# Performance work log

Measured on AMD Instinct MI355X. Metric: run time of the kernel, lower is better.

The kernel has to match this reference:

```python
import jax, jax.numpy as jnp
import numpy as np

RESO = 64
PAD = 0.1
SCALE = 8.0
PLANES = {'xz': (0, 2), 'xy': (0, 1), 'yz': (1, 2)}
PLANE_ORDER = ['xz', 'xy', 'yz']


def normalize_coordinate(p, plane):
    i, j = PLANES[plane]
    xy = jnp.stack([p[..., i], p[..., j]], axis=-1)
    xy = xy / (1.0 + PAD + 1e-3) + 0.5
    return jnp.clip(xy, 0.0, 1.0 - 1e-5)


def coordinate2index(xy, reso):
    x = (xy * reso).astype(jnp.int32)
    return x[..., 0] + reso * x[..., 1]  # (B, T)


def resblock(x, W0, b0, W1, b1, Ws):
    # ResnetBlockFC: fc_1(relu(fc_0(relu(x)))) + shortcut(x)
    net = jnp.maximum(x, 0.0) @ W0 + b0
    dx = jnp.maximum(net, 0.0) @ W1 + b1
    return x @ Ws + dx


def scatter_max_pool(c, idx_flat, num_seg):
    # c: (B, T, h); idx_flat: (B*T,) batch-offset plane indices
    B, T, h = c.shape
    pooled = jax.ops.segment_max(c.reshape(B * T, h), idx_flat, num_segments=num_seg)
    return pooled[idx_flat].reshape(B, T, h)


def plane_feature(p, c, plane):
    # scatter_mean of c into (B, c_dim, RESO, RESO); empty cells -> 0
    B, T, cd = c.shape
    R2 = RESO * RESO
    idx = coordinate2index(normalize_coordinate(p / SCALE, plane), RESO)
    idxf = (idx + jnp.arange(B, dtype=jnp.int32)[:, None] * R2).reshape(-1)
    sums = jax.ops.segment_sum(c.reshape(B * T, cd), idxf, num_segments=B * R2)
    cnt = jax.ops.segment_sum(jnp.ones((B * T,), c.dtype), idxf, num_segments=B * R2)
    mean = sums / jnp.maximum(cnt, 1.0)[:, None]
    return mean.reshape(B, R2, cd).transpose(0, 2, 1).reshape(B, cd, RESO, RESO)


def forward(p, fc_pos_W, fc_pos_b, blocks_W0, blocks_b0, blocks_W1, blocks_b1, blocks_Ws, fc_c_W, fc_c_b):
    B, T, _ = p.shape
    R2 = RESO * RESO
    offs = jnp.arange(B, dtype=jnp.int32)[:, None] * R2
    idx = {k: (coordinate2index(normalize_coordinate(p / SCALE, k), RESO) + offs).reshape(-1)
           for k in PLANE_ORDER}

    net = p @ fc_pos_W + fc_pos_b  # (B, T, 3h)
    net = resblock(net, blocks_W0[0], blocks_b0[0], blocks_W1[0], blocks_b1[0], blocks_Ws[0])
    n_blocks = blocks_W0.shape[0]
    for i in range(1, n_blocks):
        pooled = sum(scatter_max_pool(net, idx[k], B * R2) for k in PLANE_ORDER)
        meanp = jnp.broadcast_to(net.mean(axis=1, keepdims=True), net.shape)
        net = jnp.concatenate([net, pooled, meanp], axis=-1)  # (B, T, 3h)
        net = resblock(net, blocks_W0[i], blocks_b0[i], blocks_W1[i], blocks_b1[i], blocks_Ws[i])

    c = net @ fc_c_W + fc_c_b  # (B, T, c_dim)
    fea = jnp.stack([plane_feature(p, c, k) for k in PLANE_ORDER], axis=0)
    return fea  # (3, B, c_dim, RESO, RESO) in order xz, xy, yz


def setup_inputs() -> dict:
    key = jax.random.key(0)
    ks = jax.random.split(key, 10)
    B, T, dim = 16, 8192, 3
    h, c_dim, nb = 128, 128, 5
    s = 0.05
    return {
        'p': jax.random.normal(ks[0], (B, T, dim), jnp.float32) * 2.0,
        'fc_pos_W': jax.random.normal(ks[1], (dim, 3 * h), jnp.float32) * s,
        'fc_pos_b': jnp.zeros((3 * h,), jnp.float32),
        'blocks_W0': jax.random.normal(ks[2], (nb, 3 * h, h), jnp.float32) * s,
        'blocks_b0': jnp.zeros((nb, h), jnp.float32),
        'blocks_W1': jax.random.normal(ks[3], (nb, h, h), jnp.float32) * s,
        'blocks_b1': jnp.zeros((nb, h), jnp.float32),
        'blocks_Ws': jax.random.normal(ks[4], (nb, 3 * h, h), jnp.float32) * s,
        'fc_c_W': jax.random.normal(ks[5], (h, c_dim), jnp.float32) * s,
        'fc_c_b': jnp.zeros((c_dim,), jnp.float32),
    }


def reference(p, fc_pos_W, fc_pos_b, blocks_W0, blocks_b0, blocks_W1, blocks_b1, blocks_Ws, fc_c_W, fc_c_b):
    return forward(p, fc_pos_W, fc_pos_b, blocks_W0, blocks_b0, blocks_W1, blocks_b1, blocks_Ws, fc_c_W, fc_c_b)
```

## Files before the change

### kernel.cpp

```cpp
#include <hip/hip_runtime.h>

#define BT (16 * 8192)
#define NB 5
#define NCELL 65536
typedef unsigned int uint;
typedef unsigned short ushort;
typedef __attribute__((ext_vector_type(8))) short bf16x8;
typedef __attribute__((ext_vector_type(4))) float f32x4;


__device__ __forceinline__ uint f2bf(float x) {
    uint u = __float_as_uint(x);
    return (u + 0x7fffu + ((u >> 16) & 1u)) >> 16;
}
__device__ __forceinline__ float bf2f_lo(uint u) { return __uint_as_float(u << 16); }
__device__ __forceinline__ float bf2f_hi(uint u) { return __uint_as_float(u & 0xffff0000u); }
__device__ __forceinline__ uint pack2(float a, float b) { return f2bf(a) | (f2bf(b) << 16); }

__device__ __forceinline__ uint relu2(uint u) {
    uint m = (u >> 15) & 0x00010001u;
    return u & ~(m * 0xffffu);
}
__device__ __forceinline__ bf16x8 relu8(bf16x8 a) {
    uint4 u = *(uint4*)&a;
    u.x = relu2(u.x); u.y = relu2(u.y); u.z = relu2(u.z); u.w = relu2(u.w);
    return *(bf16x8*)&u;
}
__device__ __forceinline__ f32x4 bcast4(float x) { return (f32x4){x, x, x, x}; }
__device__ __forceinline__ f32x4 mfma16(bf16x8 a, bf16x8 b, f32x4 c) {
    return __builtin_amdgcn_mfma_f32_16x16x32_bf16(a, b, c, 0, 0, 0);
}

__global__ void k_idx(const float* __restrict__ p, int* __restrict__ idx) {
    int r = blockIdx.x * 256 + threadIdx.x;
    if (r >= BT) return;
    float p0 = p[3 * r + 0], p1 = p[3 * r + 1], p2 = p[3 * r + 2];
    const float DEN = (float)(1.0 + 0.1 + 1e-3);
    const float HI  = (float)(1.0 - 1e-5);
    int b = r >> 13;
    float x0 = fminf(fmaxf((p0 / 8.0f) / DEN + 0.5f, 0.0f), HI);
    float x1 = fminf(fmaxf((p1 / 8.0f) / DEN + 0.5f, 0.0f), HI);
    float x2 = fminf(fmaxf((p2 / 8.0f) / DEN + 0.5f, 0.0f), HI);
    int i0 = (int)(x0 * 64.0f);
    int i1 = (int)(x1 * 64.0f);
    int i2 = (int)(x2 * 64.0f);
    int base = b << 12;
    idx[r]          = base + i0 + (i2 << 6);
    idx[BT + r]     = base + i0 + (i1 << 6);
    idx[2 * BT + r] = base + i1 + (i2 << 6);
}

__global__ void k_hist(const int* __restrict__ idx, int* __restrict__ cnt) {
    int r = blockIdx.x * 256 + threadIdx.x;
    if (r >= BT) return;
    atomicAdd(cnt + idx[r], 1);
    atomicAdd(cnt + NCELL + idx[BT + r], 1);
    atomicAdd(cnt + 2 * NCELL + idx[2 * BT + r], 1);
}

__global__ __launch_bounds__(1024) void k_scan(const int* __restrict__ cnt,
                                               int* __restrict__ starts,
                                               int* __restrict__ cursor) {
    __shared__ int sc[1024];
    int pl = blockIdx.x, t = threadIdx.x;
    const int* c = cnt + pl * NCELL;
    int base = t * 64;
    int s = 0;
    for (int i = 0; i < 64; ++i) s += c[base + i];
    sc[t] = s;
    __syncthreads();
    for (int off = 1; off < 1024; off <<= 1) {
        int v = (t >= off) ? sc[t - off] : 0;
        __syncthreads();
        sc[t] += v;
        __syncthreads();
    }
    int run = sc[t] - s;
    for (int i = 0; i < 64; ++i) {
        int cell = base + i;
        starts[pl * NCELL + cell] = run;
        cursor[pl * NCELL + cell] = run;
        run += c[cell];
    }
}

__global__ void k_scatter_order(const int* __restrict__ idx, int* __restrict__ cursor,
                                int* __restrict__ order) {
    int r = blockIdx.x * 256 + threadIdx.x;
    if (r >= BT) return;
    for (int pl = 0; pl < 3; ++pl) {
        int cell = idx[pl * BT + r];
        int pos = atomicAdd(cursor + pl * NCELL + cell, 1);
        order[pl * BT + pos] = r;
    }
}

__global__ void k_wconv(const float* __restrict__ W0, const float* __restrict__ W1,
                        const float* __restrict__ Ws, const float* __restrict__ Wc,
                        ushort* __restrict__ wb) {
    int mat = blockIdx.y;
    int K = (mat < 5 || (mat >= 10 && mat < 15)) ? 384 : 128;
    int e = blockIdx.x * 256 + threadIdx.x;
    if (e >= K * 128) return;
    const float* src;
    size_t doff;
    if (mat < 5)       { src = W0 + (size_t)mat * 49152;        doff = (size_t)mat * 49152; }
    else if (mat < 10) { src = W1 + (size_t)(mat - 5) * 16384;  doff = 245760 + (size_t)(mat - 5) * 16384; }
    else if (mat < 15) { src = Ws + (size_t)(mat - 10) * 49152; doff = 327680 + (size_t)(mat - 10) * 49152; }
    else               { src = Wc;                              doff = 573440; }
    int ko = e & 31, n = (e >> 5) & 127, kt = e >> 12;
    wb[doff + e] = (ushort)f2bf(src[(size_t)(kt * 32 + ko) * 128 + n]);
}

__global__ __launch_bounds__(128) void k_meanvec(const float* __restrict__ meanB,
                                                 const ushort* __restrict__ wb0,
                                                 const float* __restrict__ b0v,
                                                 const ushort* __restrict__ wbs,
                                                 const float* __restrict__ b1v,
                                                 float* __restrict__ rv0,
                                                 float* __restrict__ rvS) {
    __shared__ float ms[128];
    int b = blockIdx.x, n = threadIdx.x;
    ms[n] = meanB[b * 128 + n];
    __syncthreads();
    float s0 = b0v[n], ss = b1v[n];
#pragma unroll 4
    for (int k = 0; k < 128; ++k) {
        float mv = ms[k];
        int kt = 8 + (k >> 5), ko = k & 31;
        float w0 = bf2f_lo((uint)wb0[kt * 4096 + n * 32 + ko]);
        float ws = bf2f_lo((uint)wbs[kt * 4096 + n * 32 + ko]);
        s0 = fmaf(fmaxf(mv, 0.0f), w0, s0);
        ss = fmaf(mv, ws, ss);
    }
    rv0[b * 128 + n] = s0;
    rvS[b * 128 + n] = ss;
}

__global__ __launch_bounds__(256) void k_segmax(const uint* __restrict__ netu,
                                                const int* __restrict__ starts,
                                                const int* __restrict__ cnt,
                                                const int* __restrict__ order,
                                                uint* __restrict__ segu) {
    int g = blockIdx.x * 4 + (threadIdx.x >> 6);
    int l = threadIdx.x & 63;
    int n = cnt[g];
    if (n == 0) return;
    int pl = g >> 16;
    const int* ord = order + pl * BT + starts[g];
    float m0 = -INFINITY, m1 = -INFINITY;
    int i = 0;
    for (; i + 4 <= n; i += 4) {
        uint a = netu[(size_t)ord[i] * 64 + l];
        uint b = netu[(size_t)ord[i + 1] * 64 + l];
        uint c = netu[(size_t)ord[i + 2] * 64 + l];
        uint d = netu[(size_t)ord[i + 3] * 64 + l];
        m0 = fmaxf(fmaxf(m0, fmaxf(bf2f_lo(a), bf2f_lo(b))), fmaxf(bf2f_lo(c), bf2f_lo(d)));
        m1 = fmaxf(fmaxf(m1, fmaxf(bf2f_hi(a), bf2f_hi(b))), fmaxf(bf2f_hi(c), bf2f_hi(d)));
    }
    int rem = n - i;
    if (rem > 0) {
        uint a = netu[(size_t)ord[i] * 64 + l];
        uint b = (rem > 1) ? netu[(size_t)ord[i + 1] * 64 + l] : a;
        uint c = (rem > 2) ? netu[(size_t)ord[i + 2] * 64 + l] : a;
        m0 = fmaxf(m0, fmaxf(bf2f_lo(a), fmaxf(bf2f_lo(b), bf2f_lo(c))));
        m1 = fmaxf(m1, fmaxf(bf2f_hi(a), fmaxf(bf2f_hi(b), bf2f_hi(c))));
    }
    segu[(size_t)g * 64 + l] = pack2(m0, m1);
}

template <int MODE>
__global__ __launch_bounds__(512, 6) void k_resblock(
    const float* __restrict__ p, const uint* __restrict__ netu,
    const int* __restrict__ idxg, const ushort* __restrict__ seg,
    const float* __restrict__ rv0, const float* __restrict__ rvS,
    const float* __restrict__ Wp, const float* __restrict__ bp,
    const ushort* __restrict__ wb0, const float* __restrict__ b0v,
    const ushort* __restrict__ wb1, const float* __restrict__ b1v,
    const ushort* __restrict__ wbs,
    ushort* __restrict__ out, float* __restrict__ meanW) {
    constexpr int LDA = (MODE == 0) ? 392 : 264;
    constexpr int NKT = (MODE == 0) ? 12 : 8;
    __shared__ __align__(16) ushort aT[64 * LDA];
    __shared__ __align__(16) ushort hT[64 * 136];
    const int t = threadIdx.x;
    const int rowBase = blockIdx.x * 64;
    const int bb = rowBase >> 13;

    if constexpr (MODE == 0) {
        for (int f = t; f < 3072; f += 512) {
            int row = f / 48, g = f - row * 48;
            const float* pr = p + (size_t)(rowBase + row) * 3;
            float p0 = pr[0], p1 = pr[1], p2 = pr[2];
            int k0 = g * 8;
            uint d[4];
#pragma unroll
            for (int w = 0; w < 4; ++w) {
                int k = k0 + 2 * w;
                float v0 = bp[k]     + p0 * Wp[k]     + p1 * Wp[384 + k]     + p2 * Wp[768 + k];
                float v1 = bp[k + 1] + p0 * Wp[k + 1] + p1 * Wp[384 + k + 1] + p2 * Wp[768 + k + 1];
                d[w] = pack2(v0, v1);
            }
            *(uint4*)(aT + row * LDA + k0) = make_uint4(d[0], d[1], d[2], d[3]);
        }
    } else {
        const uint4* nsrc = (const uint4*)netu;
#pragma unroll
        for (int i = 0; i < 2; ++i) {
            int f = t + 512 * i;
            int row = f >> 4, cu = f & 15;
            *(uint4*)(aT + row * LDA + cu * 8) = nsrc[(size_t)(rowBase + row) * 16 + cu];
        }
#pragma unroll
        for (int i = 0; i < 2; ++i) {
            int f = t + 512 * i;
            int row = f >> 4, grp = f & 15;
            int prow = rowBase + row;
            float o[8] = {};
#pragma unroll
            for (int pl = 0; pl < 3; ++pl) {
                int cell = idxg[pl * BT + prow];
                uint4 s4 = *(const uint4*)(seg + (size_t)(pl * NCELL + cell) * 128 + grp * 8);
                o[0] += bf2f_lo(s4.x); o[1] += bf2f_hi(s4.x);
                o[2] += bf2f_lo(s4.y); o[3] += bf2f_hi(s4.y);
                o[4] += bf2f_lo(s4.z); o[5] += bf2f_hi(s4.z);
                o[6] += bf2f_lo(s4.w); o[7] += bf2f_hi(s4.w);
            }
            uint4 d = make_uint4(pack2(o[0], o[1]), pack2(o[2], o[3]),
                                 pack2(o[4], o[5]), pack2(o[6], o[7]));
            *(uint4*)(aT + row * LDA + 128 + grp * 8) = d;
        }
    }
    __syncthreads();

    const int l = t & 63, wid = t >> 6;
    const int n0 = wid * 16;
    const int lm = l & 15, lg = l >> 4;
    const ushort* w0 = wb0 + n0 * 32;
    const ushort* w1 = wb1 + n0 * 32;
    const ushort* ws = wbs + n0 * 32;

    f32x4 acc0[4], accS[4];
    {
        float bi, si;
        if constexpr (MODE == 0) { bi = b0v[n0 + lm];            si = b1v[n0 + lm]; }
        else                     { bi = rv0[bb * 128 + n0 + lm]; si = rvS[bb * 128 + n0 + lm]; }
#pragma unroll
        for (int im = 0; im < 4; ++im) { acc0[im] = bcast4(bi); accS[im] = bcast4(si); }
    }
#pragma unroll
    for (int kt = 0; kt < NKT; ++kt) {
        bf16x8 b0 = *(const bf16x8*)(w0 + kt * 4096 + lm * 32 + lg * 8);
        bf16x8 bs = *(const bf16x8*)(ws + kt * 4096 + lm * 32 + lg * 8);
#pragma unroll
        for (int im = 0; im < 4; ++im) {
            bf16x8 a = *(const bf16x8*)(aT + (im * 16 + lm) * LDA + kt * 32 + lg * 8);
            acc0[im] = mfma16(relu8(a), b0, acc0[im]);
            accS[im] = mfma16(a, bs, accS[im]);
        }
    }
#pragma unroll
    for (int im = 0; im < 4; ++im)
#pragma unroll
        for (int j = 0; j < 4; ++j) {
            int row = im * 16 + lg * 4 + j;
            hT[row * 136 + n0 + lm] = (ushort)f2bf(fmaxf(acc0[im][j], 0.0f));
        }
    __syncthreads();

#pragma unroll
    for (int kt = 0; kt < 4; ++kt) {
        bf16x8 b = *(const bf16x8*)(w1 + kt * 4096 + lm * 32 + lg * 8);
#pragma unroll
        for (int im = 0; im < 4; ++im) {
            bf16x8 a = *(const bf16x8*)(hT + (im * 16 + lm) * 136 + kt * 32 + lg * 8);
            accS[im] = mfma16(a, b, accS[im]);
        }
    }

#pragma unroll
    for (int im = 0; im < 4; ++im)
#pragma unroll
        for (int j = 0; j < 4; ++j) {
            int row = rowBase + im * 16 + lg * 4 + j;
            out[(size_t)row * 128 + n0 + lm] = (ushort)f2bf(accS[im][j]);
        }

    if (meanW) {
        float s = 0.0f;
#pragma unroll
        for (int im = 0; im < 4; ++im)
#pragma unroll
            for (int j = 0; j < 4; ++j) s += accS[im][j];
        s += __shfl_xor(s, 16);
        s += __shfl_xor(s, 32);
        if (l < 16) atomicAdd(meanW + bb * 128 + n0 + l, s * (1.0f / 8192.0f));
    }
}

__device__ __forceinline__ void mfma_gemm3(const ushort* __restrict__ aLDS, int lda, int nk,
                                           const ushort* __restrict__ wb, int lm, int lg,
                                           f32x4 acc[4][2]) {
    for (int kt = 0; kt < nk; ++kt) {
        bf16x8 b0 = *(const bf16x8*)(wb + kt * 4096 + lm * 32 + lg * 8);
        bf16x8 b1 = *(const bf16x8*)(wb + kt * 4096 + (16 + lm) * 32 + lg * 8);
#pragma unroll
        for (int im = 0; im < 4; ++im) {
            bf16x8 a = *(const bf16x8*)(aLDS + (im * 16 + lm) * lda + kt * 32 + lg * 8);
            acc[im][0] = mfma16(a, b0, acc[im][0]);
            acc[im][1] = mfma16(a, b1, acc[im][1]);
        }
    }
}

__global__ __launch_bounds__(256, 2) void k_fcc(const uint* __restrict__ netu,
                                                const ushort* __restrict__ wbc,
                                                const float* __restrict__ bc,
                                                ushort* __restrict__ cout) {
    __shared__ __align__(16) ushort aT[64 * 136];
    const int t = threadIdx.x;
    const int rowBase = blockIdx.x * 64;
    const uint4* nsrc = (const uint4*)netu;
#pragma unroll
    for (int i = 0; i < 4; ++i) {
        int u = t + 256 * i;
        int row = u >> 4, cu = u & 15;
        *(uint4*)(aT + row * 136 + cu * 8) = nsrc[(size_t)(rowBase + row) * 16 + cu];
    }
    __syncthreads();
    const int l = t & 63, wid = t >> 6;
    const int n0 = wid * 32;
    const int lm = l & 15, lg = l >> 4;
    f32x4 acc[4][2];
    {
        float ci0 = bc[n0 + lm], ci1 = bc[n0 + 16 + lm];
#pragma unroll
        for (int im = 0; im < 4; ++im) { acc[im][0] = bcast4(ci0); acc[im][1] = bcast4(ci1); }
    }
    mfma_gemm3(aT, 136, 4, wbc + n0 * 32, lm, lg, acc);
#pragma unroll
    for (int im = 0; im < 4; ++im)
#pragma unroll
        for (int ic = 0; ic < 2; ++ic)
#pragma unroll
            for (int j = 0; j < 4; ++j) {
                int row = rowBase + im * 16 + lg * 4 + j;
                int col = n0 + ic * 16 + lm;
                cout[(size_t)row * 128 + col] = (ushort)f2bf(acc[im][ic][j]);
            }
}

__global__ __launch_bounds__(256) void k_segsum(const uint* __restrict__ cp,
                                                const int* __restrict__ starts,
                                                const int* __restrict__ cnt,
                                                const int* __restrict__ order,
                                                float* __restrict__ sums, int pl) {
    int cell = blockIdx.x * 4 + (threadIdx.x >> 6);
    int l = threadIdx.x & 63;
    int n = cnt[pl * NCELL + cell];
    if (n == 0) return;
    const int* ord = order + pl * BT + starts[pl * NCELL + cell];
    float s0 = 0.f, s1 = 0.f;
    int i = 0;
    for (; i + 4 <= n; i += 4) {
        uint a = cp[(size_t)ord[i] * 64 + l];
        uint b = cp[(size_t)ord[i + 1] * 64 + l];
        uint c = cp[(size_t)ord[i + 2] * 64 + l];
        uint d = cp[(size_t)ord[i + 3] * 64 + l];
        s0 += (bf2f_lo(a) + bf2f_lo(b)) + (bf2f_lo(c) + bf2f_lo(d));
        s1 += (bf2f_hi(a) + bf2f_hi(b)) + (bf2f_hi(c) + bf2f_hi(d));
    }
    int rem = n - i;
    if (rem > 0) {
        uint a = cp[(size_t)ord[i] * 64 + l];
        uint b = (rem > 1) ? cp[(size_t)ord[i + 1] * 64 + l] : 0u;
        uint c = (rem > 2) ? cp[(size_t)ord[i + 2] * 64 + l] : 0u;
        s0 += bf2f_lo(a) + (bf2f_lo(b) + bf2f_lo(c));
        s1 += bf2f_hi(a) + (bf2f_hi(b) + bf2f_hi(c));
    }
    *(float2*)(sums + (size_t)cell * 128 + 2 * l) = make_float2(s0, s1);
}

__global__ __launch_bounds__(256) void k_fin(const float* __restrict__ sums,
                                             const int* __restrict__ cnt,
                                             float* __restrict__ out, int pl) {
    __shared__ float tile[32][33];
    int t = threadIdx.x;
    int tx = t & 31, ty = t >> 5;
    int cl0 = (blockIdx.x & 127) << 5;
    int ch0 = (blockIdx.x >> 7) << 5;
    int b = blockIdx.y;
    int bc = b << 12;
#pragma unroll
    for (int j = 0; j < 4; ++j)
        tile[ty + 8 * j][tx] = sums[(size_t)(bc + cl0 + ty + 8 * j) * 128 + ch0 + tx];
    __syncthreads();
#pragma unroll
    for (int j = 0; j < 4; ++j) {
        int ch = ch0 + ty + 8 * j;
        int cl = cl0 + tx;
        int cn = cnt[pl * NCELL + bc + cl];
        float v = cn > 0 ? tile[tx][ty + 8 * j] / (float)cn : 0.0f;
        out[((size_t)((pl * 16 + b) * 128 + ch) << 12) + cl] = v;
    }
}

extern "C" void kernel_launch(void* const* d_in, const int* in_sizes, int n_in,
                              void* d_out, int out_size, void* d_ws, size_t ws_size,
                              hipStream_t stream) {
    const float* p  = (const float*)d_in[0];
    const float* Wp = (const float*)d_in[1];
    const float* bp = (const float*)d_in[2];
    const float* W0 = (const float*)d_in[3];
    const float* b0 = (const float*)d_in[4];
    const float* W1 = (const float*)d_in[5];
    const float* b1 = (const float*)d_in[6];
    const float* Ws = (const float*)d_in[7];
    const float* Wc = (const float*)d_in[8];
    const float* bc = (const float*)d_in[9];
    float* out = (float*)d_out;

    ushort* net    = (ushort*)d_ws;
    ushort* seg    = net + 16777216;
    float*  sums   = (float*)seg;
    ushort* wb     = seg + 25165824;
    int*    idx    = (int*)(wb + 589824);
    int*    order  = idx + 393216;
    int*    cnt    = order + 393216;
    int*    starts = cnt + 196608;
    int*    cursor = starts + 196608;
    float*  meanB  = (float*)(cursor + 196608);
    float*  rv0    = meanB + 2 * 2048;
    float*  rvS    = rv0 + 2048;

    k_idx<<<512, 256, 0, stream>>>(p, idx);
    hipMemsetAsync(cnt, 0, 3 * NCELL * 4, stream);
    k_hist<<<512, 256, 0, stream>>>(idx, cnt);
    k_scan<<<3, 1024, 0, stream>>>(cnt, starts, cursor);
    k_scatter_order<<<512, 256, 0, stream>>>(idx, cursor, order);
    k_wconv<<<dim3(192, 16), 256, 0, stream>>>(W0, W1, Ws, Wc, wb);

    hipMemsetAsync(meanB, 0, 2048 * 4, stream);
    k_resblock<0><<<2048, 512, 0, stream>>>(
        p, nullptr, nullptr, nullptr, nullptr, nullptr, Wp, bp,
        wb, b0, wb + 245760, b1, wb + 327680, net, meanB);

    for (int i = 1; i < NB; ++i) {
        const ushort* wb0i = wb + (size_t)i * 49152;
        const ushort* wb1i = wb + 245760 + (size_t)i * 16384;
        const ushort* wbsi = wb + 327680 + (size_t)i * 49152;
        k_segmax<<<49152, 256, 0, stream>>>((const uint*)net, starts, cnt, order, (uint*)seg);
        k_meanvec<<<16, 128, 0, stream>>>(meanB + ((i - 1) & 1) * 2048,
                                          wb0i, b0 + i * 128, wbsi, b1 + i * 128, rv0, rvS);
        float* mw = nullptr;
        if (i < NB - 1) {
            mw = meanB + (i & 1) * 2048;
            hipMemsetAsync(mw, 0, 2048 * 4, stream);
        }
        k_resblock<1><<<2048, 512, 0, stream>>>(
            nullptr, (const uint*)net, idx, seg, rv0, rvS, nullptr, nullptr,
            wb0i, nullptr, wb1i, nullptr, wbsi, net, mw);
    }

    k_fcc<<<2048, 256, 0, stream>>>((const uint*)net, wb + 573440, bc, net);

    for (int pl = 0; pl < 3; ++pl) {
        k_segsum<<<16384, 256, 0, stream>>>((const uint*)net, starts, cnt, order, sums, pl);
        k_fin<<<dim3(512, 16), 256, 0, stream>>>(sums, cnt, out, pl);
    }
}
```

Before: 765.1 us.

## Switch activations and weights from bf16 to fp16 with packed half ops

Replaces bf16 storage and MFMA with fp16 (16x16x32 f16 MFMA) throughout. This lets the segment-max and pooled-gather sum use packed v_pk_max_f16 and v_pk_add_f16 instead of unpacking to float and repacking. It also adds an interleaved int4 index array so the resblock gather loads all three plane cells with one 16-byte load. The trade-off is fp16's narrower range and round-toward-zero conversion, which may lose accuracy or overflow, plus an extra index write in k_idx.

After: 767.8 us. Within noise of the previous version (+0.3%).

```diff
diff --git a/kernel.cpp b/kernel.cpp
--- a/kernel.cpp
+++ b/kernel.cpp
@@ -5,33 +5,41 @@
 #define NCELL 65536
 typedef unsigned int uint;
 typedef unsigned short ushort;
-typedef __attribute__((ext_vector_type(8))) short bf16x8;
+typedef __attribute__((ext_vector_type(8))) _Float16 half8;
+typedef __attribute__((ext_vector_type(2))) __fp16 fp16x2;
+typedef __attribute__((ext_vector_type(2))) _Float16 half2v;
 typedef __attribute__((ext_vector_type(4))) float f32x4;
 
 
-__device__ __forceinline__ uint f2bf(float x) {
-    uint u = __float_as_uint(x);
-    return (u + 0x7fffu + ((u >> 16) & 1u)) >> 16;
-}
-__device__ __forceinline__ float bf2f_lo(uint u) { return __uint_as_float(u << 16); }
-__device__ __forceinline__ float bf2f_hi(uint u) { return __uint_as_float(u & 0xffff0000u); }
-__device__ __forceinline__ uint pack2(float a, float b) { return f2bf(a) | (f2bf(b) << 16); }
+__device__ __forceinline__ uint f2h2(float a, float b) {
+    fp16x2 h = __builtin_amdgcn_cvt_pkrtz(a, b);
+    return *(uint*)&h;
+}
+__device__ __forceinline__ float h2f_lo(uint u) { half2v h = *(half2v*)&u; return (float)h[0]; }
+__device__ __forceinline__ float h2f_hi(uint u) { half2v h = *(half2v*)&u; return (float)h[1]; }
+__device__ __forceinline__ uint pk_add(uint a, uint b) {
+    uint d; asm("v_pk_add_f16 %0, %1, %2" : "=v"(d) : "v"(a), "v"(b)); return d;
+}
+__device__ __forceinline__ uint pk_max(uint a, uint b) {
+    uint d; asm("v_pk_max_f16 %0, %1, %2" : "=v"(d) : "v"(a), "v"(b)); return d;
+}
 
 __device__ __forceinline__ uint relu2(uint u) {
     uint m = (u >> 15) & 0x00010001u;
     return u & ~(m * 0xffffu);
 }
-__device__ __forceinline__ bf16x8 relu8(bf16x8 a) {
+__device__ __forceinline__ half8 relu8(half8 a) {
     uint4 u = *(uint4*)&a;
     u.x = relu2(u.x); u.y = relu2(u.y); u.z = relu2(u.z); u.w = relu2(u.w);
-    return *(bf16x8*)&u;
+    return *(half8*)&u;
 }
 __device__ __forceinline__ f32x4 bcast4(float x) { return (f32x4){x, x, x, x}; }
-__device__ __forceinline__ f32x4 mfma16(bf16x8 a, bf16x8 b, f32x4 c) {
-    return __builtin_amdgcn_mfma_f32_16x16x32_bf16(a, b, c, 0, 0, 0);
-}
-
-__global__ void k_idx(const float* __restrict__ p, int* __restrict__ idx) {
+__device__ __forceinline__ f32x4 mfma16(half8 a, half8 b, f32x4 c) {
+    return __builtin_amdgcn_mfma_f32_16x16x32_f16(a, b, c, 0, 0, 0);
+}
+
+__global__ void k_idx(const float* __restrict__ p, int* __restrict__ idx,
+                      int4* __restrict__ idx4) {
     int r = blockIdx.x * 256 + threadIdx.x;
     if (r >= BT) return;
     float p0 = p[3 * r + 0], p1 = p[3 * r + 1], p2 = p[3 * r + 2];
@@ -45,9 +53,11 @@
     int i1 = (int)(x1 * 64.0f);
     int i2 = (int)(x2 * 64.0f);
     int base = b << 12;
-    idx[r]          = base + i0 + (i2 << 6);
-    idx[BT + r]     = base + i0 + (i1 << 6);
-    idx[2 * BT + r] = base + i1 + (i2 << 6);
+    int exz = base + i0 + (i2 << 6);
+    int exy = base + i0 + (i1 << 6);
+    int eyz = base + i1 + (i2 << 6);
+    idx[r] = exz; idx[BT + r] = exy; idx[2 * BT + r] = eyz;
+    idx4[r] = make_int4(exz, exy, eyz, 0);
 }
 
 __global__ void k_hist(const int* __restrict__ idx, int* __restrict__ cnt) {
@@ -109,7 +119,7 @@
     else if (mat < 15) { src = Ws + (size_t)(mat - 10) * 49152; doff = 327680 + (size_t)(mat - 10) * 49152; }
     else               { src = Wc;                              doff = 573440; }
     int ko = e & 31, n = (e >> 5) & 127, kt = e >> 12;
-    wb[doff + e] = (ushort)f2bf(src[(size_t)(kt * 32 + ko) * 128 + n]);
+    wb[doff + e] = (ushort)f2h2(src[(size_t)(kt * 32 + ko) * 128 + n], 0.0f);
 }
 
 __global__ __launch_bounds__(128) void k_meanvec(const float* __restrict__ meanB,
@@ -128,8 +138,8 @@
     for (int k = 0; k < 128; ++k) {
         float mv = ms[k];
         int kt = 8 + (k >> 5), ko = k & 31;
-        float w0 = bf2f_lo((uint)wb0[kt * 4096 + n * 32 + ko]);
-        float ws = bf2f_lo((uint)wbs[kt * 4096 + n * 32 + ko]);
+        float w0 = h2f_lo((uint)wb0[kt * 4096 + n * 32 + ko]);
+        float ws = h2f_lo((uint)wbs[kt * 4096 + n * 32 + ko]);
         s0 = fmaf(fmaxf(mv, 0.0f), w0, s0);
         ss = fmaf(mv, ws, ss);
     }
@@ -148,31 +158,29 @@
     if (n == 0) return;
     int pl = g >> 16;
     const int* ord = order + pl * BT + starts[g];
-    float m0 = -INFINITY, m1 = -INFINITY;
+    uint m = 0xFC00FC00u;
     int i = 0;
     for (; i + 4 <= n; i += 4) {
         uint a = netu[(size_t)ord[i] * 64 + l];
         uint b = netu[(size_t)ord[i + 1] * 64 + l];
         uint c = netu[(size_t)ord[i + 2] * 64 + l];
         uint d = netu[(size_t)ord[i + 3] * 64 + l];
-        m0 = fmaxf(fmaxf(m0, fmaxf(bf2f_lo(a), bf2f_lo(b))), fmaxf(bf2f_lo(c), bf2f_lo(d)));
-        m1 = fmaxf(fmaxf(m1, fmaxf(bf2f_hi(a), bf2f_hi(b))), fmaxf(bf2f_hi(c), bf2f_hi(d)));
+        m = pk_max(m, pk_max(pk_max(a, b), pk_max(c, d)));
     }
     int rem = n - i;
     if (rem > 0) {
         uint a = netu[(size_t)ord[i] * 64 + l];
         uint b = (rem > 1) ? netu[(size_t)ord[i + 1] * 64 + l] : a;
         uint c = (rem > 2) ? netu[(size_t)ord[i + 2] * 64 + l] : a;
-        m0 = fmaxf(m0, fmaxf(bf2f_lo(a), fmaxf(bf2f_lo(b), bf2f_lo(c))));
-        m1 = fmaxf(m1, fmaxf(bf2f_hi(a), fmaxf(bf2f_hi(b), bf2f_hi(c))));
-    }
-    segu[(size_t)g * 64 + l] = pack2(m0, m1);
+        m = pk_max(m, pk_max(a, pk_max(b, c)));
+    }
+    segu[(size_t)g * 64 + l] = m;
 }
 
 template <int MODE>
 __global__ __launch_bounds__(512, 6) void k_resblock(
     const float* __restrict__ p, const uint* __restrict__ netu,
-    const int* __restrict__ idxg, const ushort* __restrict__ seg,
+    const int4* __restrict__ idx4, const ushort* __restrict__ seg,
     const float* __restrict__ rv0, const float* __restrict__ rvS,
     const float* __restrict__ Wp, const float* __restrict__ bp,
     const ushort* __restrict__ wb0, const float* __restrict__ b0v,
@@ -199,7 +207,7 @@
                 int k = k0 + 2 * w;
                 float v0 = bp[k]     + p0 * Wp[k]     + p1 * Wp[384 + k]     + p2 * Wp[768 + k];
                 float v1 = bp[k + 1] + p0 * Wp[k + 1] + p1 * Wp[384 + k + 1] + p2 * Wp[768 + k + 1];
-                d[w] = pack2(v0, v1);
+                d[w] = f2h2(v0, v1);
             }
             *(uint4*)(aT + row * LDA + k0) = make_uint4(d[0], d[1], d[2], d[3]);
         }
@@ -215,19 +223,16 @@
         for (int i = 0; i < 2; ++i) {
             int f = t + 512 * i;
             int row = f >> 4, grp = f & 15;
-            int prow = rowBase + row;
-            float o[8] = {};
-#pragma unroll
-            for (int pl = 0; pl < 3; ++pl) {
-                int cell = idxg[pl * BT + prow];
-                uint4 s4 = *(const uint4*)(seg + (size_t)(pl * NCELL + cell) * 128 + grp * 8);
-                o[0] += bf2f_lo(s4.x); o[1] += bf2f_hi(s4.x);
-                o[2] += bf2f_lo(s4.y); o[3] += bf2f_hi(s4.y);
-                o[4] += bf2f_lo(s4.z); o[5] += bf2f_hi(s4.z);
-                o[6] += bf2f_lo(s4.w); o[7] += bf2f_hi(s4.w);
-            }
-            uint4 d = make_uint4(pack2(o[0], o[1]), pack2(o[2], o[3]),
-                                 pack2(o[4], o[5]), pack2(o[6], o[7]));
+            int4 cc = idx4[rowBase + row];
+            const uint4* s0 = (const uint4*)(seg + ((size_t)cc.x) * 128 + grp * 8);
+            const uint4* s1 = (const uint4*)(seg + ((size_t)NCELL + cc.y) * 128 + grp * 8);
+            const uint4* s2 = (const uint4*)(seg + ((size_t)2 * NCELL + cc.z) * 128 + grp * 8);
+            uint4 A = *s0, B = *s1, C = *s2;
+            uint4 d;
+            d.x = pk_add(pk_add(A.x, B.x), C.x);
+            d.y = pk_add(pk_add(A.y, B.y), C.y);
+            d.z = pk_add(pk_add(A.z, B.z), C.z);
+            d.w = pk_add(pk_add(A.w, B.w), C.w);
             *(uint4*)(aT + row * LDA + 128 + grp * 8) = d;
         }
     }
@@ -250,11 +255,11 @@
     }
 #pragma unroll
     for (int kt = 0; kt < NKT; ++kt) {
-        bf16x8 b0 = *(const bf16x8*)(w0 + kt * 4096 + lm * 32 + lg * 8);
-        bf16x8 bs = *(const bf16x8*)(ws + kt * 4096 + lm * 32 + lg * 8);
+        half8 b0 = *(const half8*)(w0 + kt * 4096 + lm * 32 + lg * 8);
+        half8 bs = *(const half8*)(ws + kt * 4096 + lm * 32 + lg * 8);
 #pragma unroll
         for (int im = 0; im < 4; ++im) {
-            bf16x8 a = *(const bf16x8*)(aT + (im * 16 + lm) * LDA + kt * 32 + lg * 8);
+            half8 a = *(const half8*)(aT + (im * 16 + lm) * LDA + kt * 32 + lg * 8);
             acc0[im] = mfma16(relu8(a), b0, acc0[im]);
             accS[im] = mfma16(a, bs, accS[im]);
         }
@@ -264,16 +269,16 @@
 #pragma unroll
         for (int j = 0; j < 4; ++j) {
             int row = im * 16 + lg * 4 + j;
-            hT[row * 136 + n0 + lm] = (ushort)f2bf(fmaxf(acc0[im][j], 0.0f));
+            hT[row * 136 + n0 + lm] = (ushort)f2h2(fmaxf(acc0[im][j], 0.0f), 0.0f);
         }
     __syncthreads();
 
 #pragma unroll
     for (int kt = 0; kt < 4; ++kt) {
-        bf16x8 b = *(const bf16x8*)(w1 + kt * 4096 + lm * 32 + lg * 8);
+        half8 b = *(const half8*)(w1 + kt * 4096 + lm * 32 + lg * 8);
 #pragma unroll
         for (int im = 0; im < 4; ++im) {
-            bf16x8 a = *(const bf16x8*)(hT + (im * 16 + lm) * 136 + kt * 32 + lg * 8);
+            half8 a = *(const half8*)(hT + (im * 16 + lm) * 136 + kt * 32 + lg * 8);
             accS[im] = mfma16(a, b, accS[im]);
         }
     }
@@ -283,7 +288,7 @@
 #pragma unroll
         for (int j = 0; j < 4; ++j) {
             int row = rowBase + im * 16 + lg * 4 + j;
-            out[(size_t)row * 128 + n0 + lm] = (ushort)f2bf(accS[im][j]);
+            out[(size_t)row * 128 + n0 + lm] = (ushort)f2h2(accS[im][j], 0.0f);
         }
 
     if (meanW) {
@@ -302,11 +307,11 @@
                                            const ushort* __restrict__ wb, int lm, int lg,
                                            f32x4 acc[4][2]) {
     for (int kt = 0; kt < nk; ++kt) {
-        bf16x8 b0 = *(const bf16x8*)(wb + kt * 4096 + lm * 32 + lg * 8);
-        bf16x8 b1 = *(const bf16x8*)(wb + kt * 4096 + (16 + lm) * 32 + lg * 8);
+        half8 b0 = *(const half8*)(wb + kt * 4096 + lm * 32 + lg * 8);
+        half8 b1 = *(const half8*)(wb + kt * 4096 + (16 + lm) * 32 + lg * 8);
 #pragma unroll
         for (int im = 0; im < 4; ++im) {
-            bf16x8 a = *(const bf16x8*)(aLDS + (im * 16 + lm) * lda + kt * 32 + lg * 8);
+            half8 a = *(const half8*)(aLDS + (im * 16 + lm) * lda + kt * 32 + lg * 8);
             acc[im][0] = mfma16(a, b0, acc[im][0]);
             acc[im][1] = mfma16(a, b1, acc[im][1]);
         }
@@ -346,7 +351,7 @@
             for (int j = 0; j < 4; ++j) {
                 int row = rowBase + im * 16 + lg * 4 + j;
                 int col = n0 + ic * 16 + lm;
-                cout[(size_t)row * 128 + col] = (ushort)f2bf(acc[im][ic][j]);
+                cout[(size_t)row * 128 + col] = (ushort)f2h2(acc[im][ic][j], 0.0f);
             }
 }
 
@@ -367,16 +372,16 @@
         uint b = cp[(size_t)ord[i + 1] * 64 + l];
         uint c = cp[(size_t)ord[i + 2] * 64 + l];
         uint d = cp[(size_t)ord[i + 3] * 64 + l];
-        s0 += (bf2f_lo(a) + bf2f_lo(b)) + (bf2f_lo(c) + bf2f_lo(d));
-        s1 += (bf2f_hi(a) + bf2f_hi(b)) + (bf2f_hi(c) + bf2f_hi(d));
+        s0 += (h2f_lo(a) + h2f_lo(b)) + (h2f_lo(c) + h2f_lo(d));
+        s1 += (h2f_hi(a) + h2f_hi(b)) + (h2f_hi(c) + h2f_hi(d));
     }
     int rem = n - i;
     if (rem > 0) {
         uint a = cp[(size_t)ord[i] * 64 + l];
         uint b = (rem > 1) ? cp[(size_t)ord[i + 1] * 64 + l] : 0u;
         uint c = (rem > 2) ? cp[(size_t)ord[i + 2] * 64 + l] : 0u;
-        s0 += bf2f_lo(a) + (bf2f_lo(b) + bf2f_lo(c));
-        s1 += bf2f_hi(a) + (bf2f_hi(b) + bf2f_hi(c));
+        s0 += h2f_lo(a) + (h2f_lo(b) + h2f_lo(c));
+        s1 += h2f_hi(a) + (h2f_hi(b) + h2f_hi(c));
     }
     *(float2*)(sums + (size_t)cell * 128 + 2 * l) = make_float2(s0, s1);
 }
@@ -432,15 +437,16 @@
     float*  meanB  = (float*)(cursor + 196608);
     float*  rv0    = meanB + 2 * 2048;
     float*  rvS    = rv0 + 2048;
-
-    k_idx<<<512, 256, 0, stream>>>(p, idx);
-    hipMemsetAsync(cnt, 0, 3 * NCELL * 4, stream);
+    int4*   idx4   = (int4*)(rvS + 2048);
+
+    k_idx<<<512, 256, 0, stream>>>(p, idx, idx4);
+    (void)hipMemsetAsync(cnt, 0, 3 * NCELL * 4, stream);
     k_hist<<<512, 256, 0, stream>>>(idx, cnt);
     k_scan<<<3, 1024, 0, stream>>>(cnt, starts, cursor);
     k_scatter_order<<<512, 256, 0, stream>>>(idx, cursor, order);
     k_wconv<<<dim3(192, 16), 256, 0, stream>>>(W0, W1, Ws, Wc, wb);
 
-    hipMemsetAsync(meanB, 0, 2048 * 4, stream);
+    (void)hipMemsetAsync(meanB, 0, 2048 * 4, stream);
     k_resblock<0><<<2048, 512, 0, stream>>>(
         p, nullptr, nullptr, nullptr, nullptr, nullptr, Wp, bp,
         wb, b0, wb + 245760, b1, wb + 327680, net, meanB);
@@ -455,10 +461,10 @@
         float* mw = nullptr;
         if (i < NB - 1) {
             mw = meanB + (i & 1) * 2048;
-            hipMemsetAsync(mw, 0, 2048 * 4, stream);
+            (void)hipMemsetAsync(mw, 0, 2048 * 4, stream);
         }
         k_resblock<1><<<2048, 512, 0, stream>>>(
-            nullptr, (const uint*)net, idx, seg, rv0, rvS, nullptr, nullptr,
+            nullptr, (const uint*)net, idx4, seg, rv0, rvS, nullptr, nullptr,
             wb0i, nullptr, wb1i, nullptr, wbsi, net, mw);
     }
 
```
